# Kernel optimization log

Hardware: AMD Instinct MI355X
Metric: run time of the kernel (lower is better)

Reference implementation:

```python
import jax, jax.numpy as jnp
import numpy as np

B, T, V = 16, 1024, 2048
BLANK_ID = 0
CONF_THR = 0.55
N_LABELS = 64  # alignment symbol range
FEAT = 2 * V + 4


def setup_inputs() -> dict:
    key = jax.random.key(0)
    k1, k2, k3, k4, k5 = jax.random.split(key, 5)
    shallow = jax.random.uniform(k1, (B, T, V), dtype=jnp.float32)
    final = jax.random.uniform(k2, (B, T, V), dtype=jnp.float32)
    boundary = jax.random.uniform(k3, (B, T), dtype=jnp.float32)
    align = jax.random.randint(k4, (B, T), 0, N_LABELS).astype(jnp.int64)
    lengths = jax.random.randint(k5, (B,), 1, T + 1).astype(jnp.int64)
    return {
        'shallow_posteriors': shallow,
        'final_posteriors': final,
        'boundary_probs': boundary,
        'alignments': align,
        'lengths': lengths,
    }


def _per_batch(shallow, final, boundaries, labels, length):
    # shallow/final: [T, V]; boundaries: [T]; labels: [T] int; length: scalar int
    Tn, Vn = shallow.shape
    t = jnp.arange(Tn)
    valid = t < length                                   # [T] frame validity
    lab = jnp.where(valid, labels, BLANK_ID)             # pad frames become blank runs (later dropped)
    changes = jnp.concatenate([jnp.ones((1,), bool), lab[1:] != lab[:-1]])
    run_id = jnp.cumsum(changes.astype(jnp.int32)) - 1   # run index per frame, in [0, T)
    seg_id = jnp.where(valid, run_id, Tn)                # OOB id -> dropped by segment ops
    ones = valid.astype(shallow.dtype)

    run_count = jax.ops.segment_sum(ones, seg_id, num_segments=Tn)          # frames per run
    run_start = jax.ops.segment_min(jnp.where(valid, t, Tn), seg_id, num_segments=Tn)
    run_end = jax.ops.segment_max(jnp.where(valid, t, -1), seg_id, num_segments=Tn) + 1
    run_label = lab[jnp.clip(run_start, 0, Tn - 1)]

    # per-frame label confidences
    s_lab = jnp.take_along_axis(shallow, lab[:, None].astype(jnp.int32), axis=1)[:, 0]
    f_lab = jnp.take_along_axis(final, lab[:, None].astype(jnp.int32), axis=1)[:, 0]
    fc = 0.5 * (s_lab + f_lab)
    gate = (jax.nn.sigmoid((fc - CONF_THR) * 12.0) + 0.05) * ones            # zero on pad frames
    gate_sum = jnp.maximum(jax.ops.segment_sum(gate, seg_id, num_segments=Tn), 1e-6)

    shallow_pool = jax.ops.segment_sum(shallow * gate[:, None], seg_id, num_segments=Tn) / gate_sum[:, None]
    final_pool = jax.ops.segment_sum(final * gate[:, None], seg_id, num_segments=Tn) / gate_sum[:, None]
    denom = jnp.maximum(run_count, 1.0)
    seg_conf = jax.ops.segment_sum(fc * ones, seg_id, num_segments=Tn) / denom
    s_lab_mean = jax.ops.segment_sum(s_lab * ones, seg_id, num_segments=Tn) / denom

    valid_run = (run_count > 0) & (run_label != BLANK_ID)
    rank = jnp.cumsum(valid_run.astype(jnp.int32)) - 1                       # order among nonblank segments
    is_first = rank == 0
    left_b = jnp.where(is_first, 1.0, boundaries[jnp.clip(run_start - 1, 0, Tn - 1)])
    right_b = boundaries[jnp.clip(run_end - 1, 0, Tn - 1)]
    scale = 1.0 + 0.25 * (1.0 - left_b) + 0.25 * (1.0 - right_b)

    feat = jnp.concatenate(
        [shallow_pool, final_pool,
         jnp.stack([seg_conf, s_lab_mean, left_b, right_b], axis=-1)], axis=-1
    ) * scale[:, None]                                                        # [T, 2V+4]

    out_idx = jnp.where(valid_run, rank, Tn)                                 # compact nonblank runs
    padded = jnp.zeros((Tn, FEAT), shallow.dtype).at[out_idx].set(feat, mode='drop')
    conf = jnp.zeros((Tn,), shallow.dtype).at[out_idx].set(jnp.clip(seg_conf, 0.05, 1.0), mode='drop')

    n_seg = valid_run.sum()
    conf = jnp.where((n_seg == 0) & (t == 0), 1.0, conf)                     # empty-utterance fallback
    n_out = jnp.maximum(n_seg, 1)
    return padded, n_out, conf


def reference(shallow_posteriors, final_posteriors, boundary_probs, alignments, lengths):
    padded, piece_lengths, piece_conf = jax.vmap(_per_batch)(
        shallow_posteriors, final_posteriors, boundary_probs,
        alignments.astype(jnp.int32), lengths.astype(jnp.int32))
    return padded, piece_lengths, piece_conf
```

## Files before the change

kernel.cpp:

```cpp
#include <hip/hip_runtime.h>
#include <math.h>

#define Bdim 16
#define Tdim 1024
#define Vdim 2048
#define FEAT (2 * Vdim + 4)
#define CONF_THR 0.55f

typedef float f32x4 __attribute__((ext_vector_type(4)));

struct RunMeta {
    int start;
    int end;
    float m;
    float e0, e1, e2, e3;
    float pad;
};

__global__ __launch_bounds__(1024) void phase1_kernel(
    const float* __restrict__ shallow, const float* __restrict__ final_,
    const float* __restrict__ boundary, const int* __restrict__ align,
    const int* __restrict__ lengths,
    float* __restrict__ gate_ws, RunMeta* __restrict__ meta, int* __restrict__ nseg_ws,
    float* __restrict__ out_conf, float* __restrict__ out_len)
{
    __shared__ int   s_lab[Tdim];
    __shared__ unsigned char s_change[Tdim];
    __shared__ float s_gate[Tdim];
    __shared__ float s_fc[Tdim];
    __shared__ float s_slab[Tdim];
    __shared__ int   wsum[16];
    __shared__ int   woff[16];
    __shared__ int   s_nseg;
    __shared__ int   r_start[Tdim];
    __shared__ int   r_end[Tdim];
    __shared__ int   r_label[Tdim];
    __shared__ int   r_cnt[Tdim];
    __shared__ float r_gsum[Tdim];
    __shared__ float r_fcsum[Tdim];
    __shared__ float r_ssum[Tdim];
    __shared__ float s_conf[Tdim];

    const int b = blockIdx.x;
    const int t = threadIdx.x;
    const int lane = t & 63;
    const int wid  = t >> 6;
    const int length = lengths[b];
    const bool valid = (t < length);
    const int lab = valid ? align[b * Tdim + t] : 0;
    s_lab[t] = lab;
    r_cnt[t] = 0;
    s_conf[t] = 0.0f;

    const size_t rowoff = ((size_t)(b * Tdim) + t) * Vdim;
    const float sv = shallow[rowoff + lab];
    const float fv = final_[rowoff + lab];
    __syncthreads();

    const int change = (t == 0) ? 1 : (lab != s_lab[t - 1] ? 1 : 0);
    s_change[t] = (unsigned char)change;
    {
        unsigned long long bal = __ballot(change);
        int wprefix = __popcll(bal & ((~0ULL) >> (63 - lane)));
        if (lane == 63) wsum[wid] = wprefix;

        const float fc = 0.5f * (sv + fv);
        float gate = 0.0f;
        if (valid) gate = 1.0f / (1.0f + __expf(-(fc - CONF_THR) * 12.0f)) + 0.05f;
        s_gate[t] = gate;
        s_fc[t]   = fc;
        s_slab[t] = sv;
        __syncthreads();
        if (t == 0) {
            int run = 0;
            #pragma unroll
            for (int i = 0; i < 16; ++i) { woff[i] = run; run += wsum[i]; }
        }
        __syncthreads();
        const int runid = woff[wid] + wprefix - 1;

        if (change && valid) {
            float gs = gate, fs = fc, ss = sv;
            int f = t + 1;
            while (f < length && !s_change[f]) {
                gs += s_gate[f]; fs += s_fc[f]; ss += s_slab[f]; ++f;
            }
            r_start[runid] = t;
            r_end[runid]   = f;
            r_label[runid] = lab;
            r_gsum[runid]  = gs;
            r_fcsum[runid] = fs;
            r_ssum[runid]  = ss;
            r_cnt[runid]   = f - t;
        }
    }
    __syncthreads();

    const int cnt = r_cnt[t];
    const int vr = (cnt > 0 && r_label[t] != 0) ? 1 : 0;
    unsigned long long bal2 = __ballot(vr);
    int wp2 = __popcll(bal2 & ((~0ULL) >> (63 - lane)));
    if (lane == 63) wsum[wid] = wp2;
    __syncthreads();
    if (t == 0) {
        int run = 0;
        #pragma unroll
        for (int i = 0; i < 16; ++i) { woff[i] = run; run += wsum[i]; }
        s_nseg = run;
    }
    __syncthreads();
    const int rank = woff[wid] + wp2 - 1;
    const int nseg = s_nseg;

    if (vr) {
        const int start = r_start[t];
        const int endp  = r_end[t];
        int li = start - 1; if (li < 0) li = 0;
        const float left_b  = (rank == 0) ? 1.0f : boundary[b * Tdim + li];
        const float right_b = boundary[b * Tdim + (endp - 1)];
        const float scale = 1.0f + 0.25f * (1.0f - left_b) + 0.25f * (1.0f - right_b);
        const float seg_conf  = r_fcsum[t] / (float)cnt;
        const float slab_mean = r_ssum[t] / (float)cnt;
        const float gsum = fmaxf(r_gsum[t], 1e-6f);
        RunMeta mm;
        mm.start = start;
        mm.end = endp;
        mm.m = scale / gsum;
        mm.e0 = seg_conf * scale;
        mm.e1 = slab_mean * scale;
        mm.e2 = left_b * scale;
        mm.e3 = right_b * scale;
        mm.pad = 0.f;
        meta[b * Tdim + rank] = mm;
        s_conf[rank] = fminf(fmaxf(seg_conf, 0.05f), 1.0f);
    }
    __syncthreads();
    if (t == 0) {
        if (nseg == 0) s_conf[0] = 1.0f;
        nseg_ws[b] = nseg;
        out_len[b] = (float)(nseg > 0 ? nseg : 1);
    }
    __syncthreads();
    out_conf[b * Tdim + t] = s_conf[t];
    gate_ws[b * Tdim + t] = s_gate[t];
}

__global__ __launch_bounds__(1024) void phase2_kernel(
    const float* __restrict__ shallow, const float* __restrict__ final_,
    const float* __restrict__ gate_ws, const RunMeta* __restrict__ meta,
    const int* __restrict__ nseg_ws, float* __restrict__ padded)
{
    const int tid = threadIdx.x & 255;
    const int sub = threadIdx.x >> 8;
    const int row = blockIdx.x * 4 + sub;
    const int b = row >> 10;
    const int r = row & (Tdim - 1);
    float* out = padded + (size_t)row * FEAT;
    f32x4* o4 = (f32x4*)out;
    const int ns = nseg_ws[b];

    if (r >= ns) {
        const f32x4 z = (f32x4)(0.f);
        #pragma unroll
        for (int i = 0; i < 4; ++i)
            __builtin_nontemporal_store(z, o4 + tid + 256 * i);
        if (tid == 0) __builtin_nontemporal_store(z, o4 + 1024);
        return;
    }

    const RunMeta mm = meta[row];
    f32x4 aS0 = (f32x4)(0.f), aS1 = (f32x4)(0.f), aF0 = (f32x4)(0.f), aF1 = (f32x4)(0.f);
    const f32x4* sB = (const f32x4*)(shallow + (size_t)b * Tdim * Vdim);
    const f32x4* fB = (const f32x4*)(final_  + (size_t)b * Tdim * Vdim);

    for (int f = mm.start; f < mm.end; ++f) {
        const float g = gate_ws[b * Tdim + f];
        const f32x4* srow = sB + (size_t)f * (Vdim / 4);
        const f32x4* frow = fB + (size_t)f * (Vdim / 4);
        f32x4 s0 = srow[tid];
        f32x4 s1 = srow[tid + 256];
        f32x4 f0 = frow[tid];
        f32x4 f1 = frow[tid + 256];
        aS0 += s0 * g;
        aS1 += s1 * g;
        aF0 += f0 * g;
        aF1 += f1 * g;
    }

    const float m = mm.m;
    __builtin_nontemporal_store(aS0 * m, o4 + tid);
    __builtin_nontemporal_store(aS1 * m, o4 + tid + 256);
    __builtin_nontemporal_store(aF0 * m, o4 + tid + 512);
    __builtin_nontemporal_store(aF1 * m, o4 + tid + 768);
    if (tid < 4) __builtin_nontemporal_store((&mm.e0)[tid], out + 4096 + tid);
}

extern "C" void kernel_launch(void* const* d_in, const int* in_sizes, int n_in,
                              void* d_out, int out_size, void* d_ws, size_t ws_size,
                              hipStream_t stream) {
    const float* shallow  = (const float*)d_in[0];
    const float* final_   = (const float*)d_in[1];
    const float* boundary = (const float*)d_in[2];
    const int*   align    = (const int*)d_in[3];
    const int*   lengths  = (const int*)d_in[4];

    float* out = (float*)d_out;
    float* padded   = out;
    float* out_len  = out + (size_t)Bdim * Tdim * FEAT;
    float* out_conf = out_len + Bdim;

    char* ws = (char*)d_ws;
    float* gate_ws = (float*)ws;
    int* nseg_ws = (int*)(ws + (size_t)Bdim * Tdim * sizeof(float));
    size_t meta_off = (size_t)Bdim * Tdim * sizeof(float) + 256;
    RunMeta* meta = (RunMeta*)(ws + meta_off);

    phase1_kernel<<<Bdim, Tdim, 0, stream>>>(shallow, final_, boundary, align, lengths,
                                             gate_ws, meta, nseg_ws, out_conf, out_len);
    phase2_kernel<<<(Bdim * Tdim) / 4, 1024, 0, stream>>>(shallow, final_, gate_ws, meta,
                                                          nseg_ws, padded);
}
```

Measured before the change: 75.64 us.

## Fuse run detection and segment pooling into one per-row kernel

Replaces the two-kernel pipeline with a single kernel launched with one 256-thread block per output row. Each block rebuilds the run-change and nonblank-start bitmasks for its batch in shared memory with atomicOr, then locates its run via popcount. It computes the gates inline while pooling the rows. This removes the serial per-batch phase-1 scan, the workspace round trip for gates and metadata, and one launch. In exchange, every block redundantly loads the alignment row and does bitmask scans, and each frame adds two scalar gathers for the label confidences.

New measurement: 66.67 us. -11.9%, faster.

```diff
diff --git a/kernel.cpp b/kernel.cpp
--- a/kernel.cpp
+++ b/kernel.cpp
@@ -9,190 +9,135 @@
 
 typedef float f32x4 __attribute__((ext_vector_type(4)));
 
-struct RunMeta {
-    int start;
-    int end;
-    float m;
-    float e0, e1, e2, e3;
-    float pad;
-};
-
-__global__ __launch_bounds__(1024) void phase1_kernel(
+__global__ __launch_bounds__(256) void fused_kernel(
     const float* __restrict__ shallow, const float* __restrict__ final_,
     const float* __restrict__ boundary, const int* __restrict__ align,
     const int* __restrict__ lengths,
-    float* __restrict__ gate_ws, RunMeta* __restrict__ meta, int* __restrict__ nseg_ws,
-    float* __restrict__ out_conf, float* __restrict__ out_len)
+    float* __restrict__ padded, float* __restrict__ out_len, float* __restrict__ out_conf)
 {
-    __shared__ int   s_lab[Tdim];
-    __shared__ unsigned char s_change[Tdim];
-    __shared__ float s_gate[Tdim];
-    __shared__ float s_fc[Tdim];
-    __shared__ float s_slab[Tdim];
-    __shared__ int   wsum[16];
-    __shared__ int   woff[16];
-    __shared__ int   s_nseg;
-    __shared__ int   r_start[Tdim];
-    __shared__ int   r_end[Tdim];
-    __shared__ int   r_label[Tdim];
-    __shared__ int   r_cnt[Tdim];
-    __shared__ float r_gsum[Tdim];
-    __shared__ float r_fcsum[Tdim];
-    __shared__ float r_ssum[Tdim];
-    __shared__ float s_conf[Tdim];
+    __shared__ int s_lab[Tdim];
+    __shared__ unsigned int s_chg[32];
+    __shared__ unsigned int s_nb[32];
 
-    const int b = blockIdx.x;
-    const int t = threadIdx.x;
-    const int lane = t & 63;
-    const int wid  = t >> 6;
+    const int row = blockIdx.x;
+    const int b = row >> 10;
+    const int r = row & (Tdim - 1);
+    const int tid = threadIdx.x;
     const int length = lengths[b];
-    const bool valid = (t < length);
-    const int lab = valid ? align[b * Tdim + t] : 0;
-    s_lab[t] = lab;
-    r_cnt[t] = 0;
-    s_conf[t] = 0.0f;
 
-    const size_t rowoff = ((size_t)(b * Tdim) + t) * Vdim;
-    const float sv = shallow[rowoff + lab];
-    const float fv = final_[rowoff + lab];
+    if (tid < 32) { s_chg[tid] = 0u; s_nb[tid] = 0u; }
+
+    const int4 l4 = ((const int4*)(align + b * Tdim))[tid];
+    const int t0 = tid * 4;
+    const int la0 = (t0 + 0 < length) ? l4.x : 0;
+    const int la1 = (t0 + 1 < length) ? l4.y : 0;
+    const int la2 = (t0 + 2 < length) ? l4.z : 0;
+    const int la3 = (t0 + 3 < length) ? l4.w : 0;
+    s_lab[t0 + 0] = la0; s_lab[t0 + 1] = la1;
+    s_lab[t0 + 2] = la2; s_lab[t0 + 3] = la3;
     __syncthreads();
 
-    const int change = (t == 0) ? 1 : (lab != s_lab[t - 1] ? 1 : 0);
-    s_change[t] = (unsigned char)change;
-    {
-        unsigned long long bal = __ballot(change);
-        int wprefix = __popcll(bal & ((~0ULL) >> (63 - lane)));
-        if (lane == 63) wsum[wid] = wprefix;
-
-        const float fc = 0.5f * (sv + fv);
-        float gate = 0.0f;
-        if (valid) gate = 1.0f / (1.0f + __expf(-(fc - CONF_THR) * 12.0f)) + 0.05f;
-        s_gate[t] = gate;
-        s_fc[t]   = fc;
-        s_slab[t] = sv;
-        __syncthreads();
-        if (t == 0) {
-            int run = 0;
-            #pragma unroll
-            for (int i = 0; i < 16; ++i) { woff[i] = run; run += wsum[i]; }
-        }
-        __syncthreads();
-        const int runid = woff[wid] + wprefix - 1;
-
-        if (change && valid) {
-            float gs = gate, fs = fc, ss = sv;
-            int f = t + 1;
-            while (f < length && !s_change[f]) {
-                gs += s_gate[f]; fs += s_fc[f]; ss += s_slab[f]; ++f;
-            }
-            r_start[runid] = t;
-            r_end[runid]   = f;
-            r_label[runid] = lab;
-            r_gsum[runid]  = gs;
-            r_fcsum[runid] = fs;
-            r_ssum[runid]  = ss;
-            r_cnt[runid]   = f - t;
-        }
-    }
+    const int prev = (tid == 0) ? -1 : s_lab[t0 - 1];
+    const unsigned c0 = (la0 != prev) ? 1u : 0u;
+    const unsigned c1 = (la1 != la0) ? 1u : 0u;
+    const unsigned c2 = (la2 != la1) ? 1u : 0u;
+    const unsigned c3 = (la3 != la2) ? 1u : 0u;
+    const unsigned chg = c0 | (c1 << 1) | (c2 << 2) | (c3 << 3);
+    const unsigned nb = (c0 && la0 ? 1u : 0u) | ((c1 && la1 ? 1u : 0u) << 1)
+                      | ((c2 && la2 ? 1u : 0u) << 2) | ((c3 && la3 ? 1u : 0u) << 3);
+    const unsigned sh = (tid & 7) * 4;
+    if (chg) atomicOr(&s_chg[tid >> 3], chg << sh);
+    if (nb)  atomicOr(&s_nb[tid >> 3],  nb << sh);
     __syncthreads();
 
-    const int cnt = r_cnt[t];
-    const int vr = (cnt > 0 && r_label[t] != 0) ? 1 : 0;
-    unsigned long long bal2 = __ballot(vr);
-    int wp2 = __popcll(bal2 & ((~0ULL) >> (63 - lane)));
-    if (lane == 63) wsum[wid] = wp2;
-    __syncthreads();
-    if (t == 0) {
-        int run = 0;
-        #pragma unroll
-        for (int i = 0; i < 16; ++i) { woff[i] = run; run += wsum[i]; }
-        s_nseg = run;
-    }
-    __syncthreads();
-    const int rank = woff[wid] + wp2 - 1;
-    const int nseg = s_nseg;
+    int nseg = 0;
+    #pragma unroll
+    for (int w = 0; w < 32; ++w) nseg += __popc(s_nb[w]);
 
-    if (vr) {
-        const int start = r_start[t];
-        const int endp  = r_end[t];
-        int li = start - 1; if (li < 0) li = 0;
-        const float left_b  = (rank == 0) ? 1.0f : boundary[b * Tdim + li];
-        const float right_b = boundary[b * Tdim + (endp - 1)];
-        const float scale = 1.0f + 0.25f * (1.0f - left_b) + 0.25f * (1.0f - right_b);
-        const float seg_conf  = r_fcsum[t] / (float)cnt;
-        const float slab_mean = r_ssum[t] / (float)cnt;
-        const float gsum = fmaxf(r_gsum[t], 1e-6f);
-        RunMeta mm;
-        mm.start = start;
-        mm.end = endp;
-        mm.m = scale / gsum;
-        mm.e0 = seg_conf * scale;
-        mm.e1 = slab_mean * scale;
-        mm.e2 = left_b * scale;
-        mm.e3 = right_b * scale;
-        mm.pad = 0.f;
-        meta[b * Tdim + rank] = mm;
-        s_conf[rank] = fminf(fmaxf(seg_conf, 0.05f), 1.0f);
-    }
-    __syncthreads();
-    if (t == 0) {
-        if (nseg == 0) s_conf[0] = 1.0f;
-        nseg_ws[b] = nseg;
-        out_len[b] = (float)(nseg > 0 ? nseg : 1);
-    }
-    __syncthreads();
-    out_conf[b * Tdim + t] = s_conf[t];
-    gate_ws[b * Tdim + t] = s_gate[t];
-}
-
-__global__ __launch_bounds__(1024) void phase2_kernel(
-    const float* __restrict__ shallow, const float* __restrict__ final_,
-    const float* __restrict__ gate_ws, const RunMeta* __restrict__ meta,
-    const int* __restrict__ nseg_ws, float* __restrict__ padded)
-{
-    const int tid = threadIdx.x & 255;
-    const int sub = threadIdx.x >> 8;
-    const int row = blockIdx.x * 4 + sub;
-    const int b = row >> 10;
-    const int r = row & (Tdim - 1);
     float* out = padded + (size_t)row * FEAT;
     f32x4* o4 = (f32x4*)out;
-    const int ns = nseg_ws[b];
 
-    if (r >= ns) {
+    if (r >= nseg) {
         const f32x4 z = (f32x4)(0.f);
         #pragma unroll
         for (int i = 0; i < 4; ++i)
             __builtin_nontemporal_store(z, o4 + tid + 256 * i);
-        if (tid == 0) __builtin_nontemporal_store(z, o4 + 1024);
+        if (tid == 0) {
+            __builtin_nontemporal_store(z, o4 + 1024);
+            out_conf[row] = (r == 0 && nseg == 0) ? 1.0f : 0.0f;
+            if (r == 0) out_len[b] = 1.0f;
+        }
         return;
     }
 
-    const RunMeta mm = meta[row];
-    f32x4 aS0 = (f32x4)(0.f), aS1 = (f32x4)(0.f), aF0 = (f32x4)(0.f), aF1 = (f32x4)(0.f);
-    const f32x4* sB = (const f32x4*)(shallow + (size_t)b * Tdim * Vdim);
-    const f32x4* fB = (const f32x4*)(final_  + (size_t)b * Tdim * Vdim);
-
-    for (int f = mm.start; f < mm.end; ++f) {
-        const float g = gate_ws[b * Tdim + f];
-        const f32x4* srow = sB + (size_t)f * (Vdim / 4);
-        const f32x4* frow = fB + (size_t)f * (Vdim / 4);
-        f32x4 s0 = srow[tid];
-        f32x4 s1 = srow[tid + 256];
-        f32x4 f0 = frow[tid];
-        f32x4 f1 = frow[tid + 256];
-        aS0 += s0 * g;
-        aS1 += s1 * g;
-        aF0 += f0 * g;
-        aF1 += f1 * g;
+    int start;
+    {
+        int need = r;
+        int w = 0;
+        for (; w < 32; ++w) {
+            const int c = __popc(s_nb[w]);
+            if (need < c) break;
+            need -= c;
+        }
+        unsigned word = s_nb[w];
+        for (int k = 0; k < need; ++k) word &= word - 1;
+        start = w * 32 + __ffs(word) - 1;
+    }
+    int end = Tdim;
+    {
+        const int p = start + 1;
+        int w = p >> 5;
+        if (w < 32) {
+            unsigned word = s_chg[w] & (0xFFFFFFFFu << (p & 31));
+            while (word == 0u && ++w < 32) word = s_chg[w];
+            if (word) end = w * 32 + __ffs(word) - 1;
+        }
     }
 
-    const float m = mm.m;
+    const int lab = s_lab[start];
+    const int cnt = end - start;
+    const float left_b  = (r == 0) ? 1.0f : boundary[b * Tdim + start - 1];
+    const float right_b = boundary[b * Tdim + end - 1];
+    const float scale = 1.0f + 0.25f * (1.0f - left_b) + 0.25f * (1.0f - right_b);
+
+    f32x4 aS0 = (f32x4)(0.f), aS1 = (f32x4)(0.f), aF0 = (f32x4)(0.f), aF1 = (f32x4)(0.f);
+    float gsum = 0.f, fcsum = 0.f, ssum = 0.f;
+    const float* sRow = shallow + ((size_t)(b * Tdim) + start) * Vdim;
+    const float* fRow = final_  + ((size_t)(b * Tdim) + start) * Vdim;
+
+    for (int f = 0; f < cnt; ++f) {
+        const f32x4* s4 = (const f32x4*)sRow;
+        const f32x4* f4 = (const f32x4*)fRow;
+        const float sv = sRow[lab];
+        const float fv = fRow[lab];
+        const f32x4 s0 = s4[tid];
+        const f32x4 s1 = s4[tid + 256];
+        const f32x4 f0 = f4[tid];
+        const f32x4 f1 = f4[tid + 256];
+        const float fc = 0.5f * (sv + fv);
+        const float g = 1.0f / (1.0f + __expf(-(fc - CONF_THR) * 12.0f)) + 0.05f;
+        gsum += g; fcsum += fc; ssum += sv;
+        aS0 += s0 * g; aS1 += s1 * g; aF0 += f0 * g; aF1 += f1 * g;
+        sRow += Vdim; fRow += Vdim;
+    }
+
+    const float m = scale / fmaxf(gsum, 1e-6f);
     __builtin_nontemporal_store(aS0 * m, o4 + tid);
     __builtin_nontemporal_store(aS1 * m, o4 + tid + 256);
     __builtin_nontemporal_store(aF0 * m, o4 + tid + 512);
     __builtin_nontemporal_store(aF1 * m, o4 + tid + 768);
-    if (tid < 4) __builtin_nontemporal_store((&mm.e0)[tid], out + 4096 + tid);
+    if (tid == 0) {
+        const float inv_cnt = 1.0f / (float)cnt;
+        const float seg_conf = fcsum * inv_cnt;
+        f32x4 e;
+        e.x = seg_conf * scale;
+        e.y = (ssum * inv_cnt) * scale;
+        e.z = left_b * scale;
+        e.w = right_b * scale;
+        __builtin_nontemporal_store(e, o4 + 1024);
+        out_conf[row] = fminf(fmaxf(seg_conf, 0.05f), 1.0f);
+        if (r == 0) out_len[b] = (float)nseg;
+    }
 }
 
 extern "C" void kernel_launch(void* const* d_in, const int* in_sizes, int n_in,
@@ -209,14 +154,6 @@
     float* out_len  = out + (size_t)Bdim * Tdim * FEAT;
     float* out_conf = out_len + Bdim;
 
-    char* ws = (char*)d_ws;
-    float* gate_ws = (float*)ws;
-    int* nseg_ws = (int*)(ws + (size_t)Bdim * Tdim * sizeof(float));
-    size_t meta_off = (size_t)Bdim * Tdim * sizeof(float) + 256;
-    RunMeta* meta = (RunMeta*)(ws + meta_off);
-
-    phase1_kernel<<<Bdim, Tdim, 0, stream>>>(shallow, final_, boundary, align, lengths,
-                                             gate_ws, meta, nseg_ws, out_conf, out_len);
-    phase2_kernel<<<(Bdim * Tdim) / 4, 1024, 0, stream>>>(shallow, final_, gate_ws, meta,
-                                                          nseg_ws, padded);
+    fused_kernel<<<Bdim * Tdim, 256, 0, stream>>>(shallow, final_, boundary, align,
+                                                  lengths, padded, out_len, out_conf);
 }
```
